# Kernel optimization log

Measured on AMD Instinct MI355X. Metric: run time of the kernel, lower is better.

## Reference

```python
import jax, jax.numpy as jnp
import numpy as np

IN_Q, OUT_Q = 32, 32
GRID_H, GRID_W = 64, 64
FREQ_H, FREQ_W = GRID_H, GRID_W // 2 + 1
BATCH = 32
INIT_SCALE = 0.02


def setup_inputs() -> dict:
    key = jax.random.key(0)
    keys = jax.random.split(key, 9)
    inp = {"x": jax.random.normal(keys[0], (BATCH, 4 * IN_Q, GRID_H, GRID_W), dtype=jnp.float32)}
    names = ["kr_w", "kr_x", "kr_y", "kr_z", "ki_w", "ki_x", "ki_y", "ki_z"]
    for i, n in enumerate(names):
        inp[n] = jax.random.normal(keys[i + 1], (IN_Q, OUT_Q, FREQ_H, FREQ_W), dtype=jnp.float32) * INIT_SCALE
    return inp


def reference(x, kr_w, kr_x, kr_y, kr_z, ki_w, ki_x, ki_y, ki_z):
    q = IN_Q
    # Split quaternion components and FFT each: [B, q, H, Wf] complex
    xs = jnp.stack([x[:, :q], x[:, q:2 * q], x[:, 2 * q:3 * q], x[:, 3 * q:]])  # [4,B,q,H,W]
    Xs = jnp.fft.rfft2(xs, s=(GRID_H, GRID_W), axes=(-2, -1))  # [4,B,q,H,Wf]
    # Complex kernels, stacked: [4, in_q, out_q, H, Wf]
    Ws = jnp.stack([kr_w + 1j * ki_w, kr_x + 1j * ki_x, kr_y + 1j * ki_y, kr_z + 1j * ki_z])
    # All 16 pairwise contractions in one einsum: C[p,q] = W_p contracted with X_q
    C = jnp.einsum('piohw,qbihw->pqbohw', Ws, Xs)  # [4,4,B,out,H,Wf]
    # Hamilton product combination
    Pw = C[0, 0] - C[1, 1] - C[2, 2] - C[3, 3]
    Px = C[0, 1] + C[1, 0] + C[2, 3] - C[3, 2]
    Py = C[0, 2] - C[1, 3] + C[2, 0] + C[3, 1]
    Pz = C[0, 3] + C[1, 2] - C[2, 1] + C[3, 0]
    P = jnp.stack([Pw, Px, Py, Pz])  # [4,B,out,H,Wf]
    o = jnp.fft.irfft2(P, s=(GRID_H, GRID_W), axes=(-2, -1))  # [4,B,out,H,W]
    # cat along channel dim: [B, 4*out, H, W]
    return jnp.concatenate([o[0], o[1], o[2], o[3]], axis=1)
```

## Files before the change

kernel.cpp:

```cpp
#include <hip/hip_runtime.h>

#define FH 64
#define FW 64
#define NWF 33
#define NBIN (FH*NWF)
#define NIMG 4096
#define PI2 6.283185307179586f

typedef unsigned short u16;
typedef unsigned int u32;
typedef __attribute__((ext_vector_type(8))) short bf16x8;
typedef __attribute__((ext_vector_type(8))) _Float16 f16x8;
typedef __attribute__((ext_vector_type(4))) unsigned short u16x4;
typedef __attribute__((ext_vector_type(4))) float f32x4;
typedef __attribute__((ext_vector_type(4))) int   i32x4;

__device__ __forceinline__ u16 f2bf(float f) {
    unsigned u = __float_as_uint(f);
    unsigned r = (u + 0x7FFFu + ((u >> 16) & 1u)) >> 16;
    return (u16)r;
}
__device__ __forceinline__ u16 f2h(float f) {
    _Float16 h = (_Float16)f;
    return __builtin_bit_cast(u16, h);
}
__device__ __forceinline__ float2 upk(u32 v) {
    return make_float2(__uint_as_float(v << 16), __uint_as_float(v & 0xFFFF0000u));
}
__device__ __forceinline__ u32 pk(float2 v) {
    return (u32)f2bf(v.x) | ((u32)f2bf(v.y) << 16);
}
__device__ __forceinline__ f16x8 negh(f16x8 v) {
    i32x4 t = __builtin_bit_cast(i32x4, v);
    t ^= (int)0x80008000;
    return __builtin_bit_cast(f16x8, t);
}

__global__ __launch_bounds__(256, 4) void fwd_prep_kernel(
    const float* __restrict__ x, u32* __restrict__ Xs,
    const float* __restrict__ s0, const float* __restrict__ s1,
    const float* __restrict__ s2, const float* __restrict__ s3,
    const float* __restrict__ s4, const float* __restrict__ s5,
    const float* __restrict__ s6, const float* __restrict__ s7,
    u16* __restrict__ WT)
{
    __shared__ __align__(16) u16 sm[18432];
    const int tid = threadIdx.x;

    if (blockIdx.x < 1024) {
        const int lane = tid & 63;
        const int wid  = tid >> 6;
        const int a16  = lane & 15;
        const int kg   = lane >> 4;

        u16* mats0 = sm;
        u16* mats1 = sm + 4608;
        u16* sre   = sm + 9216 + wid*2304;
        u16* sim   = sre + 1152;

        for (int t = tid; t < 4096; t += 256) {
            int a = t >> 6, bb = t & 63;
            float sn, cs;
            __sincosf(PI2 * (float)((a*bb) & 63) * (1.f/64.f), &sn, &cs);
            mats0[a*72 + bb] = f2h(cs);
            mats1[a*72 + bb] = f2h(sn);
        }
        __syncthreads();

        const int img = blockIdx.x * 4 + wid;
        const int qc = img >> 10;
        const int b  = (img >> 5) & 31;
        const int ci = img & 31;
        const float* __restrict__ src = x + ((size_t)b*128 + (size_t)qc*32 + ci) * (FH*FW);

        f16x8 xf[4][2];
        #pragma unroll
        for (int mt = 0; mt < 4; ++mt)
            #pragma unroll
            for (int ks = 0; ks < 2; ++ks) {
                const float* rp = src + (16*mt + a16)*64 + ks*32 + kg*8;
                float4 v0 = *(const float4*)rp;
                float4 v1 = *(const float4*)(rp + 4);
                xf[mt][ks] = (f16x8){ (_Float16)v0.x, (_Float16)v0.y, (_Float16)v0.z, (_Float16)v0.w,
                                      (_Float16)v1.x, (_Float16)v1.y, (_Float16)v1.z, (_Float16)v1.w };
            }

        u32* __restrict__ dst = Xs + (size_t)img * NBIN;

        #pragma unroll
        for (int nt = 0; nt < 3; ++nt) {
            f32x4 are[4], aim[4];
            #pragma unroll
            for (int mt = 0; mt < 4; ++mt) { are[mt] = (f32x4){0,0,0,0}; aim[mt] = (f32x4){0,0,0,0}; }
            #pragma unroll
            for (int ks = 0; ks < 2; ++ks) {
                const int rb = (16*nt + a16)*72 + ks*32 + kg*8;
                f16x8 cf  = *(const f16x8*)&mats0[rb];
                f16x8 nsf = negh(*(const f16x8*)&mats1[rb]);
                #pragma unroll
                for (int mt = 0; mt < 4; ++mt) {
                    are[mt] = __builtin_amdgcn_mfma_f32_16x16x32_f16(xf[mt][ks], cf,  are[mt], 0, 0, 0);
                    aim[mt] = __builtin_amdgcn_mfma_f32_16x16x32_f16(xf[mt][ks], nsf, aim[mt], 0, 0, 0);
                }
            }
            #pragma unroll
            for (int mt = 0; mt < 4; ++mt) {
                u16x4 re4 = { f2h(are[mt][0]), f2h(are[mt][1]), f2h(are[mt][2]), f2h(are[mt][3]) };
                u16x4 im4 = { f2h(aim[mt][0]), f2h(aim[mt][1]), f2h(aim[mt][2]), f2h(aim[mt][3]) };
                *(u16x4*)&sre[a16*72 + 16*mt + 4*kg] = re4;
                *(u16x4*)&sim[a16*72 + 16*mt + 4*kg] = im4;
            }
            f16x8 br[2], bi[2];
            #pragma unroll
            for (int ks = 0; ks < 2; ++ks) {
                br[ks] = *(const f16x8*)&sre[a16*72 + ks*32 + kg*8];
                bi[ks] = *(const f16x8*)&sim[a16*72 + ks*32 + kg*8];
            }
            const int k = 16*nt + a16;
            #pragma unroll
            for (int mt2 = 0; mt2 < 4; ++mt2) {
                f32x4 xre = (f32x4){0,0,0,0}, xim = (f32x4){0,0,0,0};
                #pragma unroll
                for (int ks = 0; ks < 2; ++ks) {
                    const int rb = (16*mt2 + a16)*72 + ks*32 + kg*8;
                    f16x8 cf = *(const f16x8*)&mats0[rb];
                    f16x8 sf = *(const f16x8*)&mats1[rb];
                    xre = __builtin_amdgcn_mfma_f32_16x16x32_f16(cf, br[ks], xre, 0, 0, 0);
                    xre = __builtin_amdgcn_mfma_f32_16x16x32_f16(sf, bi[ks], xre, 0, 0, 0);
                    xim = __builtin_amdgcn_mfma_f32_16x16x32_f16(cf, bi[ks], xim, 0, 0, 0);
                    xim = __builtin_amdgcn_mfma_f32_16x16x32_f16(negh(sf), br[ks], xim, 0, 0, 0);
                }
                if (k < 33) {
                    #pragma unroll
                    for (int r = 0; r < 4; ++r)
                        dst[(16*mt2 + 4*kg + r)*33 + k] = pk(make_float2(xre[r], xim[r]));
                }
            }
        }
    } else {
        const int pb = blockIdx.x - 1024;
        const int bt = pb % 66;
        const int ay = pb / 66;
        const int a  = ay >> 2;
        const int o0 = (ay & 3) * 8;
        const float* __restrict__ src =
            (a==0)?s0:(a==1)?s1:(a==2)?s2:(a==3)?s3:(a==4)?s4:(a==5)?s5:(a==6)?s6:s7;
        const int bin0 = bt * 32;
        u16* lds2 = sm;

        #pragma unroll
        for (int it = 0; it < 8; ++it) {
            int e = tid + it*256;
            int f4 = e & 7, rt = e >> 3;
            int i = rt & 31, oo = rt >> 5;
            int io = i*32 + o0 + oo;
            float4 v = ((const float4*)src)[(size_t)io*(NBIN/4) + bt*8 + f4];
            int chL = oo*32 + i;
            int bb = f4*4;
            lds2[(bb+0)*264 + chL] = f2bf(v.x);
            lds2[(bb+1)*264 + chL] = f2bf(v.y);
            lds2[(bb+2)*264 + chL] = f2bf(v.z);
            lds2[(bb+3)*264 + chL] = f2bf(v.w);
        }
        __syncthreads();
        const int p = a & 3, ri = a >> 2;
        #pragma unroll
        for (int it = 0; it < 4; ++it) {
            int e = tid + it*256;
            int binL = e >> 5, c8 = e & 31;
            bf16x8 v = *(const bf16x8*)&lds2[binL*264 + c8*8];
            size_t d = ((size_t)(bin0 + binL)*8 + p*2 + ri)*1024 + o0*32 + c8*8;
            *(bf16x8*)(WT + d) = v;
        }
    }
}

__global__ __launch_bounds__(256) void xpose_x_kernel(const u32* __restrict__ Xs,
                                                      u32* __restrict__ XT)
{
    const int g    = blockIdx.x;
    const int bin0 = blockIdx.y * 32;
    __shared__ u32 tile[32][33];
    const int tid = threadIdx.x;
    #pragma unroll
    for (int it = 0; it < 4; ++it) {
        int e = tid + it*256;
        int imgL = e >> 5, binL = e & 31;
        tile[imgL][binL] = Xs[(size_t)(g*32 + imgL) * NBIN + bin0 + binL];
    }
    __syncthreads();
    const int q = g >> 5, b = g & 31;
    #pragma unroll
    for (int it = 0; it < 2; ++it) {
        int e = tid + it*256;
        int binL = e >> 4, pr = e & 15;
        u32 v0 = tile[pr*2][binL], v1 = tile[pr*2 + 1][binL];
        u32 re = (v0 & 0xFFFFu) | (v1 << 16);
        u32 im = (v0 >> 16) | (v1 & 0xFFFF0000u);
        size_t base = ((size_t)(bin0 + binL)*8 + q*2) * 512 + b*16 + pr;
        XT[base]       = re;
        XT[base + 512] = im;
    }
}

__global__ __launch_bounds__(256) void contract_kernel(
    const u16* __restrict__ XT, const u16* __restrict__ WT,
    u32* __restrict__ P)
{
    const int bid  = blockIdx.x;
    const int bin  = (bid & 7) * (NBIN/8) + (bid >> 3);
    const int wid  = threadIdx.x >> 6;
    const int lane = threadIdx.x & 63;
    const int bh = wid >> 1, oh = wid & 1;
    const int row = lane & 15, kg = lane >> 4;

    const u16* __restrict__ xb = XT + (size_t)bin * 8192;
    const u16* __restrict__ wb = WT + (size_t)bin * 8192;

    bf16x8 ax[4][2];
    #pragma unroll
    for (int q = 0; q < 4; ++q)
        #pragma unroll
        for (int ri = 0; ri < 2; ++ri)
            ax[q][ri] = *(const bf16x8*)(xb + ((q*2 + ri)*32 + bh*16 + row)*32 + kg*8);

    bf16x8 wpos[4][2], wneg[4][2];
    #pragma unroll
    for (int p = 0; p < 4; ++p)
        #pragma unroll
        for (int ri = 0; ri < 2; ++ri) {
            bf16x8 w = *(const bf16x8*)(wb + ((p*2 + ri)*32 + oh*16 + row)*32 + kg*8);
            wpos[p][ri] = w;
            i32x4 t = __builtin_bit_cast(i32x4, w);
            t ^= (int)0x80008000;
            wneg[p][ri] = __builtin_bit_cast(bf16x8, t);
        }

    f32x4 acc[4][2];
    #pragma unroll
    for (int c = 0; c < 4; ++c)
        #pragma unroll
        for (int ri = 0; ri < 2; ++ri)
            acc[c][ri] = (f32x4){0.f, 0.f, 0.f, 0.f};

    constexpr int PI_[4][4] = {{0,1,2,3},{1,0,3,2},{2,3,0,1},{3,2,1,0}};
    constexpr int SG_[4][4] = {{1,-1,-1,-1},{1,1,-1,1},{1,1,1,-1},{1,-1,1,1}};
    #pragma unroll
    for (int c = 0; c < 4; ++c)
        #pragma unroll
        for (int q = 0; q < 4; ++q) {
            const int  p   = PI_[c][q];
            const bool pos = SG_[c][q] > 0;
            bf16x8 wr_s = pos ? wpos[p][0] : wneg[p][0];
            bf16x8 wi_s = pos ? wpos[p][1] : wneg[p][1];
            bf16x8 wi_m = pos ? wneg[p][1] : wpos[p][1];
            acc[c][0] = __builtin_amdgcn_mfma_f32_16x16x32_bf16(ax[q][0], wr_s, acc[c][0], 0, 0, 0);
            acc[c][0] = __builtin_amdgcn_mfma_f32_16x16x32_bf16(ax[q][1], wi_m, acc[c][0], 0, 0, 0);
            acc[c][1] = __builtin_amdgcn_mfma_f32_16x16x32_bf16(ax[q][1], wr_s, acc[c][1], 0, 0, 0);
            acc[c][1] = __builtin_amdgcn_mfma_f32_16x16x32_bf16(ax[q][0], wi_s, acc[c][1], 0, 0, 0);
        }

    u32* __restrict__ dst = P + (size_t)bin * 4096;
    #pragma unroll
    for (int c = 0; c < 4; ++c)
        #pragma unroll
        for (int r = 0; r < 4; ++r) {
            int b_ = bh*16 + kg*4 + r;
            int o  = oh*16 + row;
            dst[c*1024 + b_*32 + o] = pk(make_float2(acc[c][0][r], acc[c][1][r]));
        }
}

__global__ __launch_bounds__(256) void pxpose_kernel(const u32* __restrict__ P,
                                                     u32* __restrict__ PT)
{
    const int bin0 = blockIdx.x * 32;
    const int img0 = blockIdx.y * 32;
    __shared__ u32 tile[32][33];
    const int tid = threadIdx.x;
    #pragma unroll
    for (int it = 0; it < 4; ++it) {
        int e = tid + it*256;
        int bi = e >> 5, im = e & 31;
        tile[bi][im] = P[(size_t)(bin0 + bi) * 4096 + img0 + im];
    }
    __syncthreads();
    #pragma unroll
    for (int it = 0; it < 4; ++it) {
        int e = tid + it*256;
        int im = e >> 5, bi = e & 31;
        PT[(size_t)(img0 + im) * NBIN + bin0 + bi] = tile[bi][im];
    }
}

__global__ __launch_bounds__(512, 4) void fft_inv_kernel(const u32* __restrict__ PT,
                                                         float* __restrict__ out)
{
    __shared__ __align__(16) u16 mats[2][64*72];
    __shared__ __align__(16) u16 wbuf[4][7168];

    const int tid  = threadIdx.x;
    const int lane = tid & 63;
    const int wid  = tid >> 6;
    const int slot = wid >> 1;
    const int half = wid & 1;
    const int ltid = (half << 6) | lane;
    const int a16  = lane & 15;
    const int q    = lane >> 4;

    const int img = blockIdx.x * 4 + slot;
    const int c  = img >> 10;
    const int b  = (img >> 5) & 31;
    const int oc = img & 31;

    for (int t = tid; t < 4096; t += 512) {
        int a = t >> 6, bb = t & 63;
        float sn, cs;
        __sincosf(PI2 * (float)((a*bb) & 63) * (1.f/64.f), &sn, &cs);
        mats[0][a*72 + bb] = f2h(cs);
        mats[1][a*72 + bb] = f2h(sn);
    }

    u16* ETre = wbuf[slot];
    u16* ETim = wbuf[slot] + 48*72;
    for (int j = 33*72 + ltid; j < 48*72; j += 128) {
        ETre[j] = 0;
        ETim[j] = 0;
    }
    const u32* __restrict__ srcP = PT + (size_t)img * NBIN;
    for (int i = 0; i < 17; ++i) {
        int t = i*128 + ltid;
        if (t < NBIN) {
            int hf = t / 33, k = t - hf*33;
            float2 v = upk(srcP[t]);
            ETre[k*72 + hf] = f2h(v.x);
            ETim[k*72 + hf] = f2h(v.y);
        }
    }
    __syncthreads();

    f16x8 ere[2][2], eim[2][2];
    #pragma unroll
    for (int mtl = 0; mtl < 2; ++mtl) {
        const int mt = 2*half + mtl;
        if (mt < 3) {
            #pragma unroll
            for (int ks = 0; ks < 2; ++ks) {
                ere[mtl][ks] = *(const f16x8*)&ETre[(16*mt + a16)*72 + ks*32 + q*8];
                eim[mtl][ks] = *(const f16x8*)&ETim[(16*mt + a16)*72 + ks*32 + q*8];
            }
        }
    }
    __syncthreads();

    u16* Tre = wbuf[slot];
    u16* Tim = wbuf[slot] + 64*56;
    #pragma unroll
    for (int mtl = 0; mtl < 2; ++mtl) {
        const int mt = 2*half + mtl;
        if (mt < 3) {
            #pragma unroll
            for (int nt = 0; nt < 4; ++nt) {
                f32x4 tre = (f32x4){0,0,0,0}, tim = (f32x4){0,0,0,0};
                #pragma unroll
                for (int ks = 0; ks < 2; ++ks) {
                    const int rb = (16*nt + a16)*72 + ks*32 + q*8;
                    f16x8 cf = *(const f16x8*)&mats[0][rb];
                    f16x8 sf = *(const f16x8*)&mats[1][rb];
                    tre = __builtin_amdgcn_mfma_f32_16x16x32_f16(ere[mtl][ks], cf, tre, 0, 0, 0);
                    tre = __builtin_amdgcn_mfma_f32_16x16x32_f16(eim[mtl][ks], negh(sf), tre, 0, 0, 0);
                    tim = __builtin_amdgcn_mfma_f32_16x16x32_f16(ere[mtl][ks], sf, tim, 0, 0, 0);
                    tim = __builtin_amdgcn_mfma_f32_16x16x32_f16(eim[mtl][ks], cf, tim, 0, 0, 0);
                }
                const int m0 = 16*mt + 4*q;
                u16x4 r4, i4;
                #pragma unroll
                for (int r = 0; r < 4; ++r) {
                    int m = m0 + r;
                    float s = (m == 0 || m == 32) ? (1.f/4096.f) : (2.f/4096.f);
                    r4[r] = (m < 33) ? f2h(tre[r] * s) : (u16)0;
                    i4[r] = (m < 33) ? f2h(tim[r] * s) : (u16)0;
                }
                *(u16x4*)&Tre[(16*nt + a16)*56 + m0] = r4;
                *(u16x4*)&Tim[(16*nt + a16)*56 + m0] = i4;
            }
        }
    }
    __syncthreads();

    float* __restrict__ dst = out + ((size_t)b*128 + (size_t)c*32 + oc) * (FH*FW);
    #pragma unroll
    for (int mtl = 0; mtl < 2; ++mtl) {
        const int mt = 2*half + mtl;
        f16x8 tfr[2], tfi[2];
        #pragma unroll
        for (int ks = 0; ks < 2; ++ks) {
            const int mbase = ks*32 + q*8;
            if (mbase < 48) {
                tfr[ks] = *(const f16x8*)&Tre[(16*mt + a16)*56 + mbase];
                tfi[ks] = *(const f16x8*)&Tim[(16*mt + a16)*56 + mbase];
            } else {
                tfr[ks] = (f16x8){0,0,0,0,0,0,0,0};
                tfi[ks] = (f16x8){0,0,0,0,0,0,0,0};
            }
        }
        #pragma unroll
        for (int nt = 0; nt < 4; ++nt) {
            f32x4 acc = (f32x4){0,0,0,0};
            #pragma unroll
            for (int ks = 0; ks < 2; ++ks) {
                const int rb = (16*nt + a16)*72 + ks*32 + q*8;
                f16x8 cf = *(const f16x8*)&mats[0][rb];
                f16x8 sf = *(const f16x8*)&mats[1][rb];
                acc = __builtin_amdgcn_mfma_f32_16x16x32_f16(tfr[ks], cf, acc, 0, 0, 0);
                acc = __builtin_amdgcn_mfma_f32_16x16x32_f16(tfi[ks], negh(sf), acc, 0, 0, 0);
            }
            #pragma unroll
            for (int r = 0; r < 4; ++r)
                dst[(16*mt + 4*q + r)*64 + 16*nt + a16] = acc[r];
        }
    }
}

extern "C" void kernel_launch(void* const* d_in, const int* in_sizes, int n_in,
                              void* d_out, int out_size, void* d_ws, size_t ws_size,
                              hipStream_t stream)
{
    const float* x   = (const float*)d_in[0];
    const float* krw = (const float*)d_in[1];
    const float* krx = (const float*)d_in[2];
    const float* kry = (const float*)d_in[3];
    const float* krz = (const float*)d_in[4];
    const float* kiw = (const float*)d_in[5];
    const float* kix = (const float*)d_in[6];
    const float* kiy = (const float*)d_in[7];
    const float* kiz = (const float*)d_in[8];

    const size_t R = (size_t)NBIN * 8192 * sizeof(u16);
    u16* XT = (u16*)d_ws;
    u32* PT = (u32*)d_ws;
    u16* WT = (u16*)((char*)d_ws + R);
    u32* Xs = (u32*)((char*)d_ws + 2*R);
    u32* P  = Xs;
    float* out = (float*)d_out;

    fwd_prep_kernel<<<dim3(1024 + 2112), 256, 0, stream>>>(x, Xs,
                                                           krw, krx, kry, krz,
                                                           kiw, kix, kiy, kiz, WT);
    xpose_x_kernel<<<dim3(128, NBIN/32), 256, 0, stream>>>(Xs, (u32*)XT);
    contract_kernel<<<dim3(NBIN), 256, 0, stream>>>(XT, WT, P);
    pxpose_kernel<<<dim3(NBIN/32, NIMG/32), 256, 0, stream>>>(P, PT);
    fft_inv_kernel<<<dim3(NIMG/4), 512, 0, stream>>>(PT, out);
}
```

Baseline: 117.6 us.

## Fuse P transpose into inverse FFT and make forward prep persistent

Drops the separate pxpose kernel. The inverse FFT kernel now gathers its four images directly from the bin-major P buffer with strided loads into shared memory, and remaps the block index so concurrent blocks touch nearby columns. The forward prep kernel becomes a persistent 512-thread grid that interleaves FFT work items and weight-transpose items, so the twiddle tables are built once per block instead of once per work item. This removes one launch and a full round trip of P through global memory. In exchange the inverse kernel reads P with 16-byte-granular strided accesses, and the prep kernel uses more shared memory per block.

```diff
diff --git a/kernel.cpp b/kernel.cpp
--- a/kernel.cpp
+++ b/kernel.cpp
@@ -36,7 +36,7 @@
     return __builtin_bit_cast(f16x8, t);
 }
 
-__global__ __launch_bounds__(256, 4) void fwd_prep_kernel(
+__global__ __launch_bounds__(512, 4) void fwd_prep_kernel(
     const float* __restrict__ x, u32* __restrict__ Xs,
     const float* __restrict__ s0, const float* __restrict__ s1,
     const float* __restrict__ s2, const float* __restrict__ s3,
@@ -44,133 +44,136 @@
     const float* __restrict__ s6, const float* __restrict__ s7,
     u16* __restrict__ WT)
 {
-    __shared__ __align__(16) u16 sm[18432];
-    const int tid = threadIdx.x;
-
-    if (blockIdx.x < 1024) {
-        const int lane = tid & 63;
-        const int wid  = tid >> 6;
-        const int a16  = lane & 15;
-        const int kg   = lane >> 4;
-
-        u16* mats0 = sm;
-        u16* mats1 = sm + 4608;
-        u16* sre   = sm + 9216 + wid*2304;
-        u16* sim   = sre + 1152;
-
-        for (int t = tid; t < 4096; t += 256) {
-            int a = t >> 6, bb = t & 63;
-            float sn, cs;
-            __sincosf(PI2 * (float)((a*bb) & 63) * (1.f/64.f), &sn, &cs);
-            mats0[a*72 + bb] = f2h(cs);
-            mats1[a*72 + bb] = f2h(sn);
-        }
-        __syncthreads();
-
-        const int img = blockIdx.x * 4 + wid;
-        const int qc = img >> 10;
-        const int b  = (img >> 5) & 31;
-        const int ci = img & 31;
-        const float* __restrict__ src = x + ((size_t)b*128 + (size_t)qc*32 + ci) * (FH*FW);
-
-        f16x8 xf[4][2];
-        #pragma unroll
-        for (int mt = 0; mt < 4; ++mt)
-            #pragma unroll
-            for (int ks = 0; ks < 2; ++ks) {
-                const float* rp = src + (16*mt + a16)*64 + ks*32 + kg*8;
-                float4 v0 = *(const float4*)rp;
-                float4 v1 = *(const float4*)(rp + 4);
-                xf[mt][ks] = (f16x8){ (_Float16)v0.x, (_Float16)v0.y, (_Float16)v0.z, (_Float16)v0.w,
-                                      (_Float16)v1.x, (_Float16)v1.y, (_Float16)v1.z, (_Float16)v1.w };
-            }
-
-        u32* __restrict__ dst = Xs + (size_t)img * NBIN;
-
-        #pragma unroll
-        for (int nt = 0; nt < 3; ++nt) {
-            f32x4 are[4], aim[4];
-            #pragma unroll
-            for (int mt = 0; mt < 4; ++mt) { are[mt] = (f32x4){0,0,0,0}; aim[mt] = (f32x4){0,0,0,0}; }
-            #pragma unroll
-            for (int ks = 0; ks < 2; ++ks) {
-                const int rb = (16*nt + a16)*72 + ks*32 + kg*8;
-                f16x8 cf  = *(const f16x8*)&mats0[rb];
-                f16x8 nsf = negh(*(const f16x8*)&mats1[rb]);
+    __shared__ __align__(16) u16 sm[36096];
+    const int tid  = threadIdx.x;
+    const int lane = tid & 63;
+    const int wid  = tid >> 6;
+    const int a16  = lane & 15;
+    const int kg   = lane >> 4;
+
+    u16* mats0 = sm;
+    u16* mats1 = sm + 4608;
+    u16* sre   = sm + 9216 + wid*2304;
+    u16* sim   = sre + 1152;
+    u16* lds2  = sm + 27648;
+
+    for (int t = tid; t < 4096; t += 512) {
+        int a = t >> 6, bb = t & 63;
+        float sn, cs;
+        __sincosf(PI2 * (float)((a*bb) & 63) * (1.f/64.f), &sn, &cs);
+        mats0[a*72 + bb] = f2h(cs);
+        mats1[a*72 + bb] = f2h(sn);
+    }
+    __syncthreads();
+
+    for (int item = blockIdx.x; item < 2624; item += 512) {
+        const int grp = item / 41;
+        const int rem = item - grp*41;
+        if (rem < 8) {
+            const int img = (grp*8 + rem)*8 + wid;
+            const int qc = img >> 10;
+            const int b  = (img >> 5) & 31;
+            const int ci = img & 31;
+            const float* __restrict__ src = x + ((size_t)b*128 + (size_t)qc*32 + ci) * (FH*FW);
+
+            f16x8 xf[4][2];
+            #pragma unroll
+            for (int mt = 0; mt < 4; ++mt)
+                #pragma unroll
+                for (int ks = 0; ks < 2; ++ks) {
+                    const float* rp = src + (16*mt + a16)*64 + ks*32 + kg*8;
+                    float4 v0 = *(const float4*)rp;
+                    float4 v1 = *(const float4*)(rp + 4);
+                    xf[mt][ks] = (f16x8){ (_Float16)v0.x, (_Float16)v0.y, (_Float16)v0.z, (_Float16)v0.w,
+                                          (_Float16)v1.x, (_Float16)v1.y, (_Float16)v1.z, (_Float16)v1.w };
+                }
+
+            u32* __restrict__ dst = Xs + (size_t)img * NBIN;
+            #pragma unroll
+            for (int nt = 0; nt < 3; ++nt) {
+                f32x4 are[4], aim[4];
+                #pragma unroll
+                for (int mt = 0; mt < 4; ++mt) { are[mt] = (f32x4){0,0,0,0}; aim[mt] = (f32x4){0,0,0,0}; }
+                #pragma unroll
+                for (int ks = 0; ks < 2; ++ks) {
+                    const int rb = (16*nt + a16)*72 + ks*32 + kg*8;
+                    f16x8 cf  = *(const f16x8*)&mats0[rb];
+                    f16x8 nsf = negh(*(const f16x8*)&mats1[rb]);
+                    #pragma unroll
+                    for (int mt = 0; mt < 4; ++mt) {
+                        are[mt] = __builtin_amdgcn_mfma_f32_16x16x32_f16(xf[mt][ks], cf,  are[mt], 0, 0, 0);
+                        aim[mt] = __builtin_amdgcn_mfma_f32_16x16x32_f16(xf[mt][ks], nsf, aim[mt], 0, 0, 0);
+                    }
+                }
                 #pragma unroll
                 for (int mt = 0; mt < 4; ++mt) {
-                    are[mt] = __builtin_amdgcn_mfma_f32_16x16x32_f16(xf[mt][ks], cf,  are[mt], 0, 0, 0);
-                    aim[mt] = __builtin_amdgcn_mfma_f32_16x16x32_f16(xf[mt][ks], nsf, aim[mt], 0, 0, 0);
-                }
-            }
-            #pragma unroll
-            for (int mt = 0; mt < 4; ++mt) {
-                u16x4 re4 = { f2h(are[mt][0]), f2h(are[mt][1]), f2h(are[mt][2]), f2h(are[mt][3]) };
-                u16x4 im4 = { f2h(aim[mt][0]), f2h(aim[mt][1]), f2h(aim[mt][2]), f2h(aim[mt][3]) };
-                *(u16x4*)&sre[a16*72 + 16*mt + 4*kg] = re4;
-                *(u16x4*)&sim[a16*72 + 16*mt + 4*kg] = im4;
-            }
-            f16x8 br[2], bi[2];
-            #pragma unroll
-            for (int ks = 0; ks < 2; ++ks) {
-                br[ks] = *(const f16x8*)&sre[a16*72 + ks*32 + kg*8];
-                bi[ks] = *(const f16x8*)&sim[a16*72 + ks*32 + kg*8];
-            }
-            const int k = 16*nt + a16;
-            #pragma unroll
-            for (int mt2 = 0; mt2 < 4; ++mt2) {
-                f32x4 xre = (f32x4){0,0,0,0}, xim = (f32x4){0,0,0,0};
+                    u16x4 re4 = { f2h(are[mt][0]), f2h(are[mt][1]), f2h(are[mt][2]), f2h(are[mt][3]) };
+                    u16x4 im4 = { f2h(aim[mt][0]), f2h(aim[mt][1]), f2h(aim[mt][2]), f2h(aim[mt][3]) };
+                    *(u16x4*)&sre[a16*72 + 16*mt + 4*kg] = re4;
+                    *(u16x4*)&sim[a16*72 + 16*mt + 4*kg] = im4;
+                }
+                f16x8 br[2], bi[2];
                 #pragma unroll
                 for (int ks = 0; ks < 2; ++ks) {
-                    const int rb = (16*mt2 + a16)*72 + ks*32 + kg*8;
-                    f16x8 cf = *(const f16x8*)&mats0[rb];
-                    f16x8 sf = *(const f16x8*)&mats1[rb];
-                    xre = __builtin_amdgcn_mfma_f32_16x16x32_f16(cf, br[ks], xre, 0, 0, 0);
-                    xre = __builtin_amdgcn_mfma_f32_16x16x32_f16(sf, bi[ks], xre, 0, 0, 0);
-                    xim = __builtin_amdgcn_mfma_f32_16x16x32_f16(cf, bi[ks], xim, 0, 0, 0);
-                    xim = __builtin_amdgcn_mfma_f32_16x16x32_f16(negh(sf), br[ks], xim, 0, 0, 0);
-                }
-                if (k < 33) {
+                    br[ks] = *(const f16x8*)&sre[a16*72 + ks*32 + kg*8];
+                    bi[ks] = *(const f16x8*)&sim[a16*72 + ks*32 + kg*8];
+                }
+                const int k = 16*nt + a16;
+                #pragma unroll
+                for (int mt2 = 0; mt2 < 4; ++mt2) {
+                    f32x4 xre = (f32x4){0,0,0,0}, xim = (f32x4){0,0,0,0};
                     #pragma unroll
-                    for (int r = 0; r < 4; ++r)
-                        dst[(16*mt2 + 4*kg + r)*33 + k] = pk(make_float2(xre[r], xim[r]));
-                }
-            }
-        }
-    } else {
-        const int pb = blockIdx.x - 1024;
-        const int bt = pb % 66;
-        const int ay = pb / 66;
-        const int a  = ay >> 2;
-        const int o0 = (ay & 3) * 8;
-        const float* __restrict__ src =
-            (a==0)?s0:(a==1)?s1:(a==2)?s2:(a==3)?s3:(a==4)?s4:(a==5)?s5:(a==6)?s6:s7;
-        const int bin0 = bt * 32;
-        u16* lds2 = sm;
-
-        #pragma unroll
-        for (int it = 0; it < 8; ++it) {
-            int e = tid + it*256;
-            int f4 = e & 7, rt = e >> 3;
-            int i = rt & 31, oo = rt >> 5;
-            int io = i*32 + o0 + oo;
-            float4 v = ((const float4*)src)[(size_t)io*(NBIN/4) + bt*8 + f4];
-            int chL = oo*32 + i;
-            int bb = f4*4;
-            lds2[(bb+0)*264 + chL] = f2bf(v.x);
-            lds2[(bb+1)*264 + chL] = f2bf(v.y);
-            lds2[(bb+2)*264 + chL] = f2bf(v.z);
-            lds2[(bb+3)*264 + chL] = f2bf(v.w);
-        }
-        __syncthreads();
-        const int p = a & 3, ri = a >> 2;
-        #pragma unroll
-        for (int it = 0; it < 4; ++it) {
-            int e = tid + it*256;
-            int binL = e >> 5, c8 = e & 31;
-            bf16x8 v = *(const bf16x8*)&lds2[binL*264 + c8*8];
-            size_t d = ((size_t)(bin0 + binL)*8 + p*2 + ri)*1024 + o0*32 + c8*8;
-            *(bf16x8*)(WT + d) = v;
+                    for (int ks = 0; ks < 2; ++ks) {
+                        const int rb = (16*mt2 + a16)*72 + ks*32 + kg*8;
+                        f16x8 cf = *(const f16x8*)&mats0[rb];
+                        f16x8 sf = *(const f16x8*)&mats1[rb];
+                        xre = __builtin_amdgcn_mfma_f32_16x16x32_f16(cf, br[ks], xre, 0, 0, 0);
+                        xre = __builtin_amdgcn_mfma_f32_16x16x32_f16(sf, bi[ks], xre, 0, 0, 0);
+                        xim = __builtin_amdgcn_mfma_f32_16x16x32_f16(cf, bi[ks], xim, 0, 0, 0);
+                        xim = __builtin_amdgcn_mfma_f32_16x16x32_f16(negh(sf), br[ks], xim, 0, 0, 0);
+                    }
+                    if (k < 33) {
+                        #pragma unroll
+                        for (int r = 0; r < 4; ++r)
+                            dst[(16*mt2 + 4*kg + r)*33 + k] = pk(make_float2(xre[r], xim[r]));
+                    }
+                }
+            }
+        } else {
+            const int pb = grp*33 + (rem - 8);
+            const int bt = pb % 66;
+            const int ay = pb / 66;
+            const int a  = ay >> 2;
+            const int o0 = (ay & 3) * 8;
+            const float* __restrict__ src =
+                (a==0)?s0:(a==1)?s1:(a==2)?s2:(a==3)?s3:(a==4)?s4:(a==5)?s5:(a==6)?s6:s7;
+            const int bin0 = bt * 32;
+
+            #pragma unroll
+            for (int it = 0; it < 4; ++it) {
+                int e = tid + it*512;
+                int f4 = e & 7, rt = e >> 3;
+                int i = rt & 31, oo = rt >> 5;
+                int io = i*32 + o0 + oo;
+                float4 v = ((const float4*)src)[(size_t)io*(NBIN/4) + bt*8 + f4];
+                int chL = oo*32 + i;
+                int bb = f4*4;
+                lds2[(bb+0)*264 + chL] = f2bf(v.x);
+                lds2[(bb+1)*264 + chL] = f2bf(v.y);
+                lds2[(bb+2)*264 + chL] = f2bf(v.z);
+                lds2[(bb+3)*264 + chL] = f2bf(v.w);
+            }
+            __syncthreads();
+            const int p = a & 3, ri = a >> 2;
+            #pragma unroll
+            for (int it = 0; it < 2; ++it) {
+                int e = tid + it*512;
+                int binL = e >> 5, c8 = e & 31;
+                bf16x8 v = *(const bf16x8*)&lds2[binL*264 + c8*8];
+                size_t d = ((size_t)(bin0 + binL)*8 + p*2 + ri)*1024 + o0*32 + c8*8;
+                *(bf16x8*)(WT + d) = v;
+            }
+            __syncthreads();
         }
     }
 }
@@ -271,29 +274,7 @@
         }
 }
 
-__global__ __launch_bounds__(256) void pxpose_kernel(const u32* __restrict__ P,
-                                                     u32* __restrict__ PT)
-{
-    const int bin0 = blockIdx.x * 32;
-    const int img0 = blockIdx.y * 32;
-    __shared__ u32 tile[32][33];
-    const int tid = threadIdx.x;
-    #pragma unroll
-    for (int it = 0; it < 4; ++it) {
-        int e = tid + it*256;
-        int bi = e >> 5, im = e & 31;
-        tile[bi][im] = P[(size_t)(bin0 + bi) * 4096 + img0 + im];
-    }
-    __syncthreads();
-    #pragma unroll
-    for (int it = 0; it < 4; ++it) {
-        int e = tid + it*256;
-        int im = e >> 5, bi = e & 31;
-        PT[(size_t)(img0 + im) * NBIN + bin0 + bi] = tile[bi][im];
-    }
-}
-
-__global__ __launch_bounds__(512, 4) void fft_inv_kernel(const u32* __restrict__ PT,
+__global__ __launch_bounds__(512, 4) void fft_inv_kernel(const u32* __restrict__ P,
                                                          float* __restrict__ out)
 {
     __shared__ __align__(16) u16 mats[2][64*72];
@@ -308,7 +289,9 @@
     const int a16  = lane & 15;
     const int q    = lane >> 4;
 
-    const int img = blockIdx.x * 4 + slot;
+    const int bid = blockIdx.x;
+    const int g   = (bid & 7) * 128 + (bid >> 3);
+    const int img = g * 4 + slot;
     const int c  = img >> 10;
     const int b  = (img >> 5) & 31;
     const int oc = img & 31;
@@ -321,24 +304,28 @@
         mats[1][a*72 + bb] = f2h(sn);
     }
 
+    {
+        u16* ETre = wbuf[slot];
+        u16* ETim = wbuf[slot] + 48*72;
+        for (int j = 33*72 + ltid; j < 48*72; j += 128) {
+            ETre[j] = 0;
+            ETim[j] = 0;
+        }
+    }
+    for (int e = tid; e < NBIN*4; e += 512) {
+        int bin = e >> 2, sl = e & 3;
+        u32 v = P[(size_t)bin * 4096 + g*4 + sl];
+        float2 f = upk(v);
+        int hf = bin / 33, k = bin - hf*33;
+        u16* ETre = wbuf[sl];
+        u16* ETim = wbuf[sl] + 48*72;
+        ETre[k*72 + hf] = f2h(f.x);
+        ETim[k*72 + hf] = f2h(f.y);
+    }
+    __syncthreads();
+
     u16* ETre = wbuf[slot];
     u16* ETim = wbuf[slot] + 48*72;
-    for (int j = 33*72 + ltid; j < 48*72; j += 128) {
-        ETre[j] = 0;
-        ETim[j] = 0;
-    }
-    const u32* __restrict__ srcP = PT + (size_t)img * NBIN;
-    for (int i = 0; i < 17; ++i) {
-        int t = i*128 + ltid;
-        if (t < NBIN) {
-            int hf = t / 33, k = t - hf*33;
-            float2 v = upk(srcP[t]);
-            ETre[k*72 + hf] = f2h(v.x);
-            ETim[k*72 + hf] = f2h(v.y);
-        }
-    }
-    __syncthreads();
-
     f16x8 ere[2][2], eim[2][2];
     #pragma unroll
     for (int mtl = 0; mtl < 2; ++mtl) {
@@ -438,17 +425,15 @@
 
     const size_t R = (size_t)NBIN * 8192 * sizeof(u16);
     u16* XT = (u16*)d_ws;
-    u32* PT = (u32*)d_ws;
     u16* WT = (u16*)((char*)d_ws + R);
     u32* Xs = (u32*)((char*)d_ws + 2*R);
     u32* P  = Xs;
     float* out = (float*)d_out;
 
-    fwd_prep_kernel<<<dim3(1024 + 2112), 256, 0, stream>>>(x, Xs,
-                                                           krw, krx, kry, krz,
-                                                           kiw, kix, kiy, kiz, WT);
+    fwd_prep_kernel<<<dim3(512), 512, 0, stream>>>(x, Xs,
+                                                   krw, krx, kry, krz,
+                                                   kiw, kix, kiy, kiz, WT);
     xpose_x_kernel<<<dim3(128, NBIN/32), 256, 0, stream>>>(Xs, (u32*)XT);
     contract_kernel<<<dim3(NBIN), 256, 0, stream>>>(XT, WT, P);
-    pxpose_kernel<<<dim3(NBIN/32, NIMG/32), 256, 0, stream>>>(P, PT);
-    fft_inv_kernel<<<dim3(NIMG/4), 512, 0, stream>>>(PT, out);
-}
+    fft_inv_kernel<<<dim3(NIMG/4), 512, 0, stream>>>(P, out);
+}
```

Measured after the change: 124.8 us. 6.1% more time.
